# Kernel optimization log

Hardware: AMD Instinct MI355X
Metric: run time of the kernel (lower is better)

## Reference

```python
import jax, jax.numpy as jnp
import numpy as np

N_AGENTS = 32
STATE_DIM = 512
EMBED = 64
BATCH = 32768


def setup_inputs() -> dict:
    key = jax.random.key(0)
    ks = jax.random.split(key, 16)
    g = lambda k, shape, fan_in: jax.random.normal(k, shape, jnp.float32) / np.sqrt(fan_in)
    return {
        "agent_qs": jax.random.normal(ks[0], (BATCH, N_AGENTS), jnp.float32),
        "states": jax.random.normal(ks[1], (BATCH, STATE_DIM), jnp.float32),
        # hyper_w1: Linear(state,E) -> ReLU -> Linear(E, n_agents*E)
        "w1_l1_w": g(ks[2], (EMBED, STATE_DIM), STATE_DIM),
        "w1_l1_b": jnp.zeros((EMBED,), jnp.float32),
        "w1_l2_w": g(ks[3], (N_AGENTS * EMBED, EMBED), EMBED),
        "w1_l2_b": jnp.zeros((N_AGENTS * EMBED,), jnp.float32),
        # hyper_w2: Linear(state,E) -> ReLU -> Linear(E, E)
        "w2_l1_w": g(ks[4], (EMBED, STATE_DIM), STATE_DIM),
        "w2_l1_b": jnp.zeros((EMBED,), jnp.float32),
        "w2_l2_w": g(ks[5], (EMBED, EMBED), EMBED),
        "w2_l2_b": jnp.zeros((EMBED,), jnp.float32),
        # hyper_b1: Linear(state, E)
        "b1_w": g(ks[6], (EMBED, STATE_DIM), STATE_DIM),
        "b1_b": jnp.zeros((EMBED,), jnp.float32),
        # hyper_b2: Linear(state,E) -> ReLU -> Linear(E, 1)
        "b2_l1_w": g(ks[7], (EMBED, STATE_DIM), STATE_DIM),
        "b2_l1_b": jnp.zeros((EMBED,), jnp.float32),
        "b2_l2_w": g(ks[8], (1, EMBED), EMBED),
        "b2_l2_b": jnp.zeros((1,), jnp.float32),
    }


def _linear(x, w, b):
    return x @ w.T + b


def reference(agent_qs, states,
              w1_l1_w, w1_l1_b, w1_l2_w, w1_l2_b,
              w2_l1_w, w2_l1_b, w2_l2_w, w2_l2_b,
              b1_w, b1_b, b2_l1_w, b2_l1_b, b2_l2_w, b2_l2_b):
    B = agent_qs.shape[0]
    # hypernetworks producing per-sample weights
    w1 = jnp.abs(_linear(jax.nn.relu(_linear(states, w1_l1_w, w1_l1_b)), w1_l2_w, w1_l2_b))
    w1 = w1.reshape(B, N_AGENTS, EMBED)                      # [B, A, E]
    b1 = _linear(states, b1_w, b1_b)                         # [B, E]
    hidden = jax.nn.elu(jnp.einsum('ba,bae->be', agent_qs, w1) + b1)  # [B, E]
    w2 = jnp.abs(_linear(jax.nn.relu(_linear(states, w2_l1_w, w2_l1_b)), w2_l2_w, w2_l2_b))  # [B, E]
    b2 = _linear(jax.nn.relu(_linear(states, b2_l1_w, b2_l1_b)), b2_l2_w, b2_l2_b)           # [B, 1]
    q_total = jnp.einsum('be,be->b', hidden, w2) + b2[:, 0]  # [B]
    return q_total
```

## Files before the change

kernel.cpp:

```cpp
#include <hip/hip_runtime.h>

typedef unsigned short u16;
typedef unsigned int u32;
typedef short bf16x8 __attribute__((ext_vector_type(8)));
typedef float f32x4 __attribute__((ext_vector_type(4)));
typedef u16 u16x4 __attribute__((ext_vector_type(4)));

#define NAG 32
#define STATE 512
#define EMBED 64
#define TB 64

#define OFF_W1L1 0
#define OFF_W2L1 32768
#define OFF_B1W  65536
#define OFF_B2L1 98304
#define OFF_W1L2 131072
#define OFF_W2L2 262144
#define WS_TOTAL 266240

__device__ __forceinline__ float bf2f(u16 u) {
    u32 i = ((u32)u) << 16; float f;
    __builtin_memcpy(&f, &i, 4); return f;
}
__device__ __forceinline__ u16 f2bf(float f) {
    u32 i; __builtin_memcpy(&i, &f, 4);
    return (u16)((i + 0x8000u) >> 16);
}
__device__ __forceinline__ bf16x8 ld8(const u16* p) {
    return *reinterpret_cast<const bf16x8*>(p);
}
__device__ __forceinline__ bf16x8 cvt8(f32x4 a, f32x4 b) {
    bf16x8 r;
#pragma unroll
    for (int i = 0; i < 4; ++i) r[i]     = (short)f2bf(a[i]);
#pragma unroll
    for (int i = 0; i < 4; ++i) r[i + 4] = (short)f2bf(b[i]);
    return r;
}
__device__ __forceinline__ void dma16(const void* g, void* l) {
    __builtin_amdgcn_global_load_lds(
        (const __attribute__((address_space(1))) u32*)g,
        (__attribute__((address_space(3))) u32*)l, 16, 0, 0);
}

__global__ __launch_bounds__(256) void cvt_weights(
    const float* __restrict__ w1l1w, const float* __restrict__ w2l1w,
    const float* __restrict__ b1w,   const float* __restrict__ b2l1w,
    const float* __restrict__ w1l2w, const float* __restrict__ w2l2w,
    u16* __restrict__ ws)
{
    int idx = blockIdx.x * 256 + threadIdx.x;
    const float* src; int off;
    if      (idx < OFF_W2L1)  { src = w1l1w; off = OFF_W1L1; }
    else if (idx < OFF_B1W)   { src = w2l1w; off = OFF_W2L1; }
    else if (idx < OFF_B2L1)  { src = b1w;   off = OFF_B1W;  }
    else if (idx < OFF_W1L2)  { src = b2l1w; off = OFF_B2L1; }
    else if (idx < OFF_W2L2)  { src = w1l2w; off = OFF_W1L2; }
    else if (idx < WS_TOTAL)  { src = w2l2w; off = OFF_W2L2; }
    else return;
    ws[idx] = f2bf(src[idx - off]);
}

__global__ __launch_bounds__(256, 2) void qmix_kernel(
    const float* __restrict__ qs,    const float* __restrict__ st,
    const u16*  __restrict__ wsb,
    const float* __restrict__ w1l1b, const float* __restrict__ w1l2b,
    const float* __restrict__ w2l1b, const float* __restrict__ w2l2b,
    const float* __restrict__ b1b,   const float* __restrict__ b2l1b,
    const float* __restrict__ b2l2w, const float* __restrict__ b2l2b,
    float* __restrict__ out)
{
    __shared__ u16  wbuf[256 * 64];
    __shared__ u16  y[TB][264];
    __shared__ u16  qslb[TB][40];
    __shared__ u16  w1bs[2048];
    __shared__ float qacc[TB];
    __shared__ float b2wv[64];

    const int t    = threadIdx.x;
    const int wave = t >> 6, lane = t & 63;
    const int m = lane & 15, quad = lane >> 4;
    const int sbase = blockIdx.x * TB;
    const int s0 = wave * 16;

    if (t < 64) b2wv[t] = b2l2w[t];
    {
        f32x4 q0 = *reinterpret_cast<const f32x4*>(qs + (size_t)sbase * NAG + t * 8);
        f32x4 q1 = *reinterpret_cast<const f32x4*>(qs + (size_t)sbase * NAG + t * 8 + 4);
        *reinterpret_cast<bf16x8*>(&qslb[t >> 2][(t & 3) * 8]) = cvt8(q0, q1);
        f32x4 w0 = *reinterpret_cast<const f32x4*>(w1l2b + t * 8);
        f32x4 w1 = *reinterpret_cast<const f32x4*>(w1l2b + t * 8 + 4);
        *reinterpret_cast<bf16x8*>(&w1bs[t * 8]) = cvt8(w0, w1);
    }

    float abias[16];
#pragma unroll
    for (int tt = 0; tt < 4; ++tt) abias[tt]      = w1l1b[tt * 16 + m];
#pragma unroll
    for (int tt = 0; tt < 4; ++tt) abias[tt + 4]  = w2l1b[tt * 16 + m];
#pragma unroll
    for (int tt = 0; tt < 4; ++tt) abias[tt + 8]  = b1b[tt * 16 + m];
#pragma unroll
    for (int tt = 0; tt < 4; ++tt) abias[tt + 12] = b2l1b[tt * 16 + m];

    const float* astB = st + (size_t)(sbase + s0 + m) * STATE + quad * 8;
    const int rsub = lane >> 3, cch = lane & 7;

    f32x4 acc[16] = {};
    for (int ksl = 0; ksl < 8; ++ksl) {
        __syncthreads();
#pragma unroll
        for (int j = 0; j < 8; ++j) {
            const int row = wave * 64 + j * 8 + rsub;
            const int sc  = cch ^ (row & 7);
            dma16(wsb + (size_t)row * STATE + ksl * 64 + sc * 8,
                  &wbuf[(wave * 64 + j * 8) * 64 + lane * 8]);
        }
        f32x4 av0 = *reinterpret_cast<const f32x4*>(astB + ksl * 64);
        f32x4 av1 = *reinterpret_cast<const f32x4*>(astB + ksl * 64 + 4);
        f32x4 av2 = *reinterpret_cast<const f32x4*>(astB + ksl * 64 + 32);
        f32x4 av3 = *reinterpret_cast<const f32x4*>(astB + ksl * 64 + 36);
        __builtin_amdgcn_s_waitcnt(0);
        __syncthreads();
        bf16x8 af0 = cvt8(av0, av1);
        bf16x8 af1 = cvt8(av2, av3);
#pragma unroll
        for (int tt = 0; tt < 16; ++tt) {
            const int brow = tt * 16 + m;
            bf16x8 b0 = ld8(&wbuf[brow * 64 + ((quad) ^ (brow & 7)) * 8]);
            acc[tt] = __builtin_amdgcn_mfma_f32_16x16x32_bf16(af0, b0, acc[tt], 0, 0, 0);
        }
#pragma unroll
        for (int tt = 0; tt < 16; ++tt) {
            const int brow = tt * 16 + m;
            bf16x8 b1 = ld8(&wbuf[brow * 64 + ((4 + quad) ^ (brow & 7)) * 8]);
            acc[tt] = __builtin_amdgcn_mfma_f32_16x16x32_bf16(af1, b1, acc[tt], 0, 0, 0);
        }
    }
#pragma unroll
    for (int tt = 0; tt < 16; ++tt) {
        const bool isrelu = (tt < 8) || (tt >= 12);
        const int fcol = tt * 16 + m;
#pragma unroll
        for (int r = 0; r < 4; ++r) {
            float v = acc[tt][r] + abias[tt];
            if (isrelu) v = fmaxf(v, 0.f);
            y[s0 + quad * 4 + r][fcol] = f2bf(v);
        }
    }
    __syncthreads();

    bf16x8 haf0 = *reinterpret_cast<const bf16x8*>(&y[s0 + m][quad * 8]);
    bf16x8 haf1 = *reinterpret_cast<const bf16x8*>(&y[s0 + m][32 + quad * 8]);

    f32x4 hacc[4] = {};
    for (int bs = 0; bs < 8; ++bs) {
        __syncthreads();
#pragma unroll
        for (int j = 0; j < 8; ++j) {
            const int row = wave * 64 + j * 8 + rsub;
            const int sc  = cch ^ (row & 7);
            dma16(wsb + OFF_W1L2 + ((size_t)bs * 256 + row) * EMBED + sc * 8,
                  &wbuf[(wave * 64 + j * 8) * 64 + lane * 8]);
        }
        u16x4 qv4[4];
#pragma unroll
        for (int r = 0; r < 4; ++r)
            qv4[r] = *reinterpret_cast<const u16x4*>(&qslb[s0 + quad * 4 + r][bs * 4]);
        __builtin_amdgcn_s_waitcnt(0);
        __syncthreads();
#pragma unroll
        for (int aloc = 0; aloc < 4; ++aloc) {
#pragma unroll
            for (int tp = 0; tp < 4; ++tp) {
                const int row = aloc * 64 + tp * 16 + m;
                bf16x8 b0 = ld8(&wbuf[row * 64 + ((quad) ^ (row & 7)) * 8]);
                bf16x8 b1 = ld8(&wbuf[row * 64 + ((4 + quad) ^ (row & 7)) * 8]);
                f32x4 p = {};
                p = __builtin_amdgcn_mfma_f32_16x16x32_bf16(haf0, b0, p, 0, 0, 0);
                p = __builtin_amdgcn_mfma_f32_16x16x32_bf16(haf1, b1, p, 0, 0, 0);
                const float bias = bf2f(w1bs[(bs * 4 + aloc) * EMBED + tp * 16 + m]);
#pragma unroll
                for (int r = 0; r < 4; ++r)
                    hacc[tp][r] += bf2f((u16)qv4[r][aloc]) * fabsf(p[r] + bias);
            }
        }
    }
    __syncthreads();
    u16* hid = wbuf;
#pragma unroll
    for (int tp = 0; tp < 4; ++tp) {
#pragma unroll
        for (int r = 0; r < 4; ++r) {
            const int s = s0 + quad * 4 + r, e = tp * 16 + m;
            float v = hacc[tp][r] + bf2f(y[s][128 + e]);
            v = (v > 0.f) ? v : (__expf(v) - 1.f);
            hid[s * 66 + e] = f2bf(v);
        }
    }
    __syncthreads();

    bf16x8 h2f0 = *reinterpret_cast<const bf16x8*>(&y[s0 + m][64 + quad * 8]);
    bf16x8 h2f1 = *reinterpret_cast<const bf16x8*>(&y[s0 + m][96 + quad * 8]);

    f32x4 qp = {};
#pragma unroll
    for (int tp = 0; tp < 4; ++tp) {
        const u16* wc = wsb + OFF_W2L2 + (size_t)(tp * 16 + m) * EMBED + quad * 8;
        bf16x8 b0 = ld8(wc);
        bf16x8 b1 = ld8(wc + 32);
        f32x4 p = {};
        p = __builtin_amdgcn_mfma_f32_16x16x32_bf16(h2f0, b0, p, 0, 0, 0);
        p = __builtin_amdgcn_mfma_f32_16x16x32_bf16(h2f1, b1, p, 0, 0, 0);
        const float bias = w2l2b[tp * 16 + m];
#pragma unroll
        for (int r = 0; r < 4; ++r)
            qp[r] += bf2f(hid[(s0 + quad * 4 + r) * 66 + tp * 16 + m]) * fabsf(p[r] + bias);
    }
#pragma unroll
    for (int off = 1; off < 16; off <<= 1) {
#pragma unroll
        for (int r = 0; r < 4; ++r) qp[r] += __shfl_xor(qp[r], off, 64);
    }
    if (m == 0) {
#pragma unroll
        for (int r = 0; r < 4; ++r) qacc[s0 + quad * 4 + r] = qp[r];
    }
    __syncthreads();

    if (t < TB) {
        float q = qacc[t] + b2l2b[0];
        float acc2 = 0.f;
#pragma unroll
        for (int kk = 0; kk < 8; ++kk) {
            bf16x8 hv = *reinterpret_cast<const bf16x8*>(&y[t][192 + kk * 8]);
#pragma unroll
            for (int j = 0; j < 8; ++j)
                acc2 += bf2f((u16)hv[j]) * b2wv[kk * 8 + j];
        }
        out[sbase + t] = q + acc2;
    }
}

extern "C" void kernel_launch(void* const* d_in, const int* in_sizes, int n_in,
                              void* d_out, int out_size, void* d_ws, size_t ws_size,
                              hipStream_t stream)
{
    const float* qs    = (const float*)d_in[0];
    const float* st    = (const float*)d_in[1];
    const float* w1l1w = (const float*)d_in[2];
    const float* w1l1b = (const float*)d_in[3];
    const float* w1l2w = (const float*)d_in[4];
    const float* w1l2b = (const float*)d_in[5];
    const float* w2l1w = (const float*)d_in[6];
    const float* w2l1b = (const float*)d_in[7];
    const float* w2l2w = (const float*)d_in[8];
    const float* w2l2b = (const float*)d_in[9];
    const float* b1w   = (const float*)d_in[10];
    const float* b1b   = (const float*)d_in[11];
    const float* b2l1w = (const float*)d_in[12];
    const float* b2l1b = (const float*)d_in[13];
    const float* b2l2w = (const float*)d_in[14];
    const float* b2l2b = (const float*)d_in[15];

    u16* wsb = (u16*)d_ws;

    cvt_weights<<<(WS_TOTAL + 255) / 256, 256, 0, stream>>>(
        w1l1w, w2l1w, b1w, b2l1w, w1l2w, w2l2w, wsb);

    int B = in_sizes[0] / NAG;
    int grid = B / TB;
    qmix_kernel<<<grid, 256, 0, stream>>>(
        qs, st, wsb,
        w1l1b, w1l2b, w2l1b, w2l2b, b1b, b2l1b, b2l2w, b2l2b,
        (float*)d_out);
}
```

Measured before the change: 146.8 us.

## Split hypernet GEMMs by output columns per wave, load weights from registers

Changes the work split. Each wave now computes one 64-column hypernet output for all 64 samples instead of 16 samples across all 256 columns. The wave loads weight fragments straight from global memory into registers, replacing the LDS DMA staging and its per-iteration barriers. The w1_l2 mixing stage is split by agent across waves, and the four partial sums are reduced through a new LDS buffer before the ELU. This removes block-wide syncs and LDS weight traffic, at the cost of re-reading the state from global memory four times per block, more registers (a 4x4 accumulator array), and an extra bf16 rounding of the partial sums.

Result: slower. 175.3 us (+19.4%).

```diff
diff --git a/kernel.cpp b/kernel.cpp
--- a/kernel.cpp
+++ b/kernel.cpp
@@ -37,11 +37,6 @@
 #pragma unroll
     for (int i = 0; i < 4; ++i) r[i + 4] = (short)f2bf(b[i]);
     return r;
-}
-__device__ __forceinline__ void dma16(const void* g, void* l) {
-    __builtin_amdgcn_global_load_lds(
-        (const __attribute__((address_space(1))) u32*)g,
-        (__attribute__((address_space(3))) u32*)l, 16, 0, 0);
 }
 
 __global__ __launch_bounds__(256) void cvt_weights(
@@ -71,9 +66,9 @@
     const float* __restrict__ b2l2w, const float* __restrict__ b2l2b,
     float* __restrict__ out)
 {
-    __shared__ u16  wbuf[256 * 64];
     __shared__ u16  y[TB][264];
-    __shared__ u16  qslb[TB][40];
+    __shared__ u16  pbuf[4][TB][68];
+    __shared__ u16  qst[NAG][68];
     __shared__ u16  w1bs[2048];
     __shared__ float qacc[TB];
     __shared__ float b2wv[64];
@@ -82,125 +77,147 @@
     const int wave = t >> 6, lane = t & 63;
     const int m = lane & 15, quad = lane >> 4;
     const int sbase = blockIdx.x * TB;
-    const int s0 = wave * 16;
 
     if (t < 64) b2wv[t] = b2l2w[t];
     {
-        f32x4 q0 = *reinterpret_cast<const f32x4*>(qs + (size_t)sbase * NAG + t * 8);
-        f32x4 q1 = *reinterpret_cast<const f32x4*>(qs + (size_t)sbase * NAG + t * 8 + 4);
-        *reinterpret_cast<bf16x8*>(&qslb[t >> 2][(t & 3) * 8]) = cvt8(q0, q1);
+        const float* qp = qs + (size_t)sbase * NAG + t * 8;
+        f32x4 q0 = *reinterpret_cast<const f32x4*>(qp);
+        f32x4 q1 = *reinterpret_cast<const f32x4*>(qp + 4);
+        const int s = t >> 2, a0 = (t & 3) * 8;
+#pragma unroll
+        for (int j = 0; j < 4; ++j) qst[a0 + j][s]     = f2bf(q0[j]);
+#pragma unroll
+        for (int j = 0; j < 4; ++j) qst[a0 + 4 + j][s] = f2bf(q1[j]);
         f32x4 w0 = *reinterpret_cast<const f32x4*>(w1l2b + t * 8);
         f32x4 w1 = *reinterpret_cast<const f32x4*>(w1l2b + t * 8 + 4);
         *reinterpret_cast<bf16x8*>(&w1bs[t * 8]) = cvt8(w0, w1);
     }
 
-    float abias[16];
-#pragma unroll
-    for (int tt = 0; tt < 4; ++tt) abias[tt]      = w1l1b[tt * 16 + m];
-#pragma unroll
-    for (int tt = 0; tt < 4; ++tt) abias[tt + 4]  = w2l1b[tt * 16 + m];
-#pragma unroll
-    for (int tt = 0; tt < 4; ++tt) abias[tt + 8]  = b1b[tt * 16 + m];
-#pragma unroll
-    for (int tt = 0; tt < 4; ++tt) abias[tt + 12] = b2l1b[tt * 16 + m];
-
-    const float* astB = st + (size_t)(sbase + s0 + m) * STATE + quad * 8;
-    const int rsub = lane >> 3, cch = lane & 7;
-
-    f32x4 acc[16] = {};
-    for (int ksl = 0; ksl < 8; ++ksl) {
-        __syncthreads();
+    const u16*   wArow = wsb + (size_t)(wave * 64) * STATE;
+    const float* stb   = st + (size_t)sbase * STATE;
+
+    f32x4 acc[4][4] = {};
+    for (int ks = 0; ks < 8; ++ks) {
+        bf16x8 b[4][2];
+#pragma unroll
+        for (int ot = 0; ot < 4; ++ot) {
+            const u16* wr = wArow + (size_t)(ot * 16 + m) * STATE + ks * 64 + quad * 8;
+            b[ot][0] = ld8(wr);
+            b[ot][1] = ld8(wr + 32);
+        }
+#pragma unroll
+        for (int st2 = 0; st2 < 4; ++st2) {
+            const float* ap = stb + (size_t)(st2 * 16 + m) * STATE + ks * 64 + quad * 8;
+            f32x4 a0 = *reinterpret_cast<const f32x4*>(ap);
+            f32x4 a1 = *reinterpret_cast<const f32x4*>(ap + 4);
+            f32x4 a2 = *reinterpret_cast<const f32x4*>(ap + 32);
+            f32x4 a3 = *reinterpret_cast<const f32x4*>(ap + 36);
+            bf16x8 af0 = cvt8(a0, a1);
+            bf16x8 af1 = cvt8(a2, a3);
+#pragma unroll
+            for (int ot = 0; ot < 4; ++ot)
+                acc[st2][ot] = __builtin_amdgcn_mfma_f32_16x16x32_bf16(af0, b[ot][0], acc[st2][ot], 0, 0, 0);
+#pragma unroll
+            for (int ot = 0; ot < 4; ++ot)
+                acc[st2][ot] = __builtin_amdgcn_mfma_f32_16x16x32_bf16(af1, b[ot][1], acc[st2][ot], 0, 0, 0);
+        }
+    }
+    {
+        const float* barr = (wave == 0) ? w1l1b : (wave == 1) ? w2l1b : (wave == 2) ? b1b : b2l1b;
+        const bool isrelu = (wave != 2);
+        float wb[4];
+#pragma unroll
+        for (int ot = 0; ot < 4; ++ot) wb[ot] = barr[ot * 16 + m];
+#pragma unroll
+        for (int st2 = 0; st2 < 4; ++st2)
+#pragma unroll
+            for (int ot = 0; ot < 4; ++ot)
+#pragma unroll
+                for (int r = 0; r < 4; ++r) {
+                    float v = acc[st2][ot][r] + wb[ot];
+                    if (isrelu) v = fmaxf(v, 0.f);
+                    y[st2 * 16 + quad * 4 + r][wave * 64 + ot * 16 + m] = f2bf(v);
+                }
+    }
+    __syncthreads();
+
+    bf16x8 h1f[4][2];
+#pragma unroll
+    for (int st2 = 0; st2 < 4; ++st2) {
+        h1f[st2][0] = *reinterpret_cast<const bf16x8*>(&y[st2 * 16 + m][quad * 8]);
+        h1f[st2][1] = *reinterpret_cast<const bf16x8*>(&y[st2 * 16 + m][32 + quad * 8]);
+    }
+
+    f32x4 hacc[4][4] = {};
+    for (int ag = 0; ag < 8; ++ag) {
+        const int a = wave * 8 + ag;
+        const u16* wp = wsb + OFF_W1L2 + (size_t)a * 64 * EMBED;
+        bf16x8 b[4][2];
+#pragma unroll
+        for (int ot = 0; ot < 4; ++ot) {
+            const u16* wr = wp + (size_t)(ot * 16 + m) * EMBED + quad * 8;
+            b[ot][0] = ld8(wr);
+            b[ot][1] = ld8(wr + 32);
+        }
+        float bias[4];
+#pragma unroll
+        for (int ot = 0; ot < 4; ++ot) bias[ot] = bf2f(w1bs[a * EMBED + ot * 16 + m]);
+#pragma unroll
+        for (int st2 = 0; st2 < 4; ++st2) {
+            u16x4 qv = *reinterpret_cast<const u16x4*>(&qst[a][st2 * 16 + quad * 4]);
+#pragma unroll
+            for (int ot = 0; ot < 4; ++ot) {
+                f32x4 p = {};
+                p = __builtin_amdgcn_mfma_f32_16x16x32_bf16(h1f[st2][0], b[ot][0], p, 0, 0, 0);
+                p = __builtin_amdgcn_mfma_f32_16x16x32_bf16(h1f[st2][1], b[ot][1], p, 0, 0, 0);
+#pragma unroll
+                for (int r = 0; r < 4; ++r)
+                    hacc[st2][ot][r] += bf2f((u16)qv[r]) * fabsf(p[r] + bias[ot]);
+            }
+        }
+    }
+#pragma unroll
+    for (int st2 = 0; st2 < 4; ++st2)
+#pragma unroll
+        for (int ot = 0; ot < 4; ++ot)
+#pragma unroll
+            for (int r = 0; r < 4; ++r)
+                pbuf[wave][st2 * 16 + quad * 4 + r][ot * 16 + m] = f2bf(hacc[st2][ot][r]);
+    __syncthreads();
+
+    {
+        const int s  = wave * 16 + (lane & 15);
+        const int eb = (lane >> 4) * 16;
+        float v[16];
+#pragma unroll
+        for (int j = 0; j < 16; ++j) v[j] = 0.f;
+#pragma unroll
+        for (int pw = 0; pw < 4; ++pw) {
+#pragma unroll
+            for (int c = 0; c < 4; ++c) {
+                u16x4 x = *reinterpret_cast<const u16x4*>(&pbuf[pw][s][eb + c * 4]);
+#pragma unroll
+                for (int j = 0; j < 4; ++j) v[c * 4 + j] += bf2f((u16)x[j]);
+            }
+        }
+        bf16x8 bv0 = *reinterpret_cast<const bf16x8*>(&y[s][128 + eb]);
+        bf16x8 bv1 = *reinterpret_cast<const bf16x8*>(&y[s][128 + eb + 8]);
+        bf16x8 o0, o1;
 #pragma unroll
         for (int j = 0; j < 8; ++j) {
-            const int row = wave * 64 + j * 8 + rsub;
-            const int sc  = cch ^ (row & 7);
-            dma16(wsb + (size_t)row * STATE + ksl * 64 + sc * 8,
-                  &wbuf[(wave * 64 + j * 8) * 64 + lane * 8]);
-        }
-        f32x4 av0 = *reinterpret_cast<const f32x4*>(astB + ksl * 64);
-        f32x4 av1 = *reinterpret_cast<const f32x4*>(astB + ksl * 64 + 4);
-        f32x4 av2 = *reinterpret_cast<const f32x4*>(astB + ksl * 64 + 32);
-        f32x4 av3 = *reinterpret_cast<const f32x4*>(astB + ksl * 64 + 36);
-        __builtin_amdgcn_s_waitcnt(0);
-        __syncthreads();
-        bf16x8 af0 = cvt8(av0, av1);
-        bf16x8 af1 = cvt8(av2, av3);
-#pragma unroll
-        for (int tt = 0; tt < 16; ++tt) {
-            const int brow = tt * 16 + m;
-            bf16x8 b0 = ld8(&wbuf[brow * 64 + ((quad) ^ (brow & 7)) * 8]);
-            acc[tt] = __builtin_amdgcn_mfma_f32_16x16x32_bf16(af0, b0, acc[tt], 0, 0, 0);
-        }
-#pragma unroll
-        for (int tt = 0; tt < 16; ++tt) {
-            const int brow = tt * 16 + m;
-            bf16x8 b1 = ld8(&wbuf[brow * 64 + ((4 + quad) ^ (brow & 7)) * 8]);
-            acc[tt] = __builtin_amdgcn_mfma_f32_16x16x32_bf16(af1, b1, acc[tt], 0, 0, 0);
-        }
-    }
-#pragma unroll
-    for (int tt = 0; tt < 16; ++tt) {
-        const bool isrelu = (tt < 8) || (tt >= 12);
-        const int fcol = tt * 16 + m;
-#pragma unroll
-        for (int r = 0; r < 4; ++r) {
-            float v = acc[tt][r] + abias[tt];
-            if (isrelu) v = fmaxf(v, 0.f);
-            y[s0 + quad * 4 + r][fcol] = f2bf(v);
-        }
-    }
-    __syncthreads();
-
-    bf16x8 haf0 = *reinterpret_cast<const bf16x8*>(&y[s0 + m][quad * 8]);
-    bf16x8 haf1 = *reinterpret_cast<const bf16x8*>(&y[s0 + m][32 + quad * 8]);
-
-    f32x4 hacc[4] = {};
-    for (int bs = 0; bs < 8; ++bs) {
-        __syncthreads();
-#pragma unroll
-        for (int j = 0; j < 8; ++j) {
-            const int row = wave * 64 + j * 8 + rsub;
-            const int sc  = cch ^ (row & 7);
-            dma16(wsb + OFF_W1L2 + ((size_t)bs * 256 + row) * EMBED + sc * 8,
-                  &wbuf[(wave * 64 + j * 8) * 64 + lane * 8]);
-        }
-        u16x4 qv4[4];
-#pragma unroll
-        for (int r = 0; r < 4; ++r)
-            qv4[r] = *reinterpret_cast<const u16x4*>(&qslb[s0 + quad * 4 + r][bs * 4]);
-        __builtin_amdgcn_s_waitcnt(0);
-        __syncthreads();
-#pragma unroll
-        for (int aloc = 0; aloc < 4; ++aloc) {
-#pragma unroll
-            for (int tp = 0; tp < 4; ++tp) {
-                const int row = aloc * 64 + tp * 16 + m;
-                bf16x8 b0 = ld8(&wbuf[row * 64 + ((quad) ^ (row & 7)) * 8]);
-                bf16x8 b1 = ld8(&wbuf[row * 64 + ((4 + quad) ^ (row & 7)) * 8]);
-                f32x4 p = {};
-                p = __builtin_amdgcn_mfma_f32_16x16x32_bf16(haf0, b0, p, 0, 0, 0);
-                p = __builtin_amdgcn_mfma_f32_16x16x32_bf16(haf1, b1, p, 0, 0, 0);
-                const float bias = bf2f(w1bs[(bs * 4 + aloc) * EMBED + tp * 16 + m]);
-#pragma unroll
-                for (int r = 0; r < 4; ++r)
-                    hacc[tp][r] += bf2f((u16)qv4[r][aloc]) * fabsf(p[r] + bias);
-            }
-        }
-    }
-    __syncthreads();
-    u16* hid = wbuf;
-#pragma unroll
-    for (int tp = 0; tp < 4; ++tp) {
-#pragma unroll
-        for (int r = 0; r < 4; ++r) {
-            const int s = s0 + quad * 4 + r, e = tp * 16 + m;
-            float v = hacc[tp][r] + bf2f(y[s][128 + e]);
-            v = (v > 0.f) ? v : (__expf(v) - 1.f);
-            hid[s * 66 + e] = f2bf(v);
-        }
-    }
-    __syncthreads();
-
+            float h0 = v[j] + bf2f((u16)bv0[j]);
+            h0 = (h0 > 0.f) ? h0 : (__expf(h0) - 1.f);
+            o0[j] = (short)f2bf(h0);
+            float h1 = v[8 + j] + bf2f((u16)bv1[j]);
+            h1 = (h1 > 0.f) ? h1 : (__expf(h1) - 1.f);
+            o1[j] = (short)f2bf(h1);
+        }
+        *reinterpret_cast<bf16x8*>(&y[s][128 + eb])     = o0;
+        *reinterpret_cast<bf16x8*>(&y[s][128 + eb + 8]) = o1;
+    }
+    __syncthreads();
+
+    const int s0 = wave * 16;
     bf16x8 h2f0 = *reinterpret_cast<const bf16x8*>(&y[s0 + m][64 + quad * 8]);
     bf16x8 h2f1 = *reinterpret_cast<const bf16x8*>(&y[s0 + m][96 + quad * 8]);
 
@@ -216,7 +233,7 @@
         const float bias = w2l2b[tp * 16 + m];
 #pragma unroll
         for (int r = 0; r < 4; ++r)
-            qp[r] += bf2f(hid[(s0 + quad * 4 + r) * 66 + tp * 16 + m]) * fabsf(p[r] + bias);
+            qp[r] += bf2f(y[s0 + quad * 4 + r][128 + tp * 16 + m]) * fabsf(p[r] + bias);
     }
 #pragma unroll
     for (int off = 1; off < 16; off <<= 1) {
```
